# Kernel tuning notes

Hardware: AMD Instinct MI355X
Metric: run time of the kernel (lower is better)

The kernel has to match this reference:

```python
import jax, jax.numpy as jnp
import numpy as np

K_BINS = 8192
HIDDEN = 2048
SQRT2 = 1.4142135623730951
LEAKY_SLOPE = 0.01
TMIN = 1e-10


def setup_inputs() -> dict:
    key = jax.random.key(0)
    k0, k1, k2 = jax.random.split(key, 3)
    D = 2 * K_BINS  # mu length so that cat([mu, t]) has 2K+1 features
    # positive mu keeps mu ** (gamma - 1/(1-gamma)) (a fractional power) finite
    mu = jax.random.uniform(k0, (D,), jnp.float32, 0.1, 1.0)
    t = jnp.array([0.5], jnp.float32)
    gamma = jnp.array([0.5], jnp.float32)  # 1/(1-gamma) = 2 -> integral exponent
    W1 = jax.random.normal(k1, (D + 1, HIDDEN), jnp.float32) * (1.0 / np.sqrt(D + 1))
    b1 = jnp.zeros((HIDDEN,), jnp.float32)
    W2 = jax.random.normal(k2, (HIDDEN, D), jnp.float32) * (1.0 / np.sqrt(HIDDEN))
    b2 = jnp.zeros((D,), jnp.float32)
    return {"mu": mu, "t": t, "gamma": gamma, "W1": W1, "b1": b1,
            "W2": W2, "b2": b2, "K": K_BINS}


def reference(mu, t, gamma, W1, b1, W2, b2, K):
    g = gamma[0]
    # --- NN(cat([mu, t])) -> (mu_epsilon, ln_sigma_epsilon), each [K] ---
    inp = jnp.concatenate([mu, t])                      # [2K+1]
    h = jax.nn.leaky_relu(inp @ W1 + b1, LEAKY_SLOPE)   # [hidden]
    out = h @ W2 + b2                                   # [2K]
    mu_eps, ln_sig = out[:K], out[K:]
    # --- mu_x / sigma_x (t < tmin branch folded in via where) ---
    p_mu = g - 1.0 / (1.0 - g)
    p_eps = 1.0 / (1.0 - g)
    mu_x_nn = jnp.power(mu[:K], p_mu) * jnp.power(mu_eps, p_eps)
    sigma_x_nn = jnp.power(1.0 - g, -0.5) * jnp.exp(0.5 * ln_sig)
    use_nn = t[0] >= TMIN
    mu_x = jnp.where(use_nn, mu_x_nn, jnp.zeros_like(mu_eps))     # [K]
    sigma_x = jnp.where(use_nn, sigma_x_nn, jnp.ones_like(mu_eps))  # [K]
    # --- vectorized discretised CDF differences over the (D_out, K) grid ---
    kk = jnp.arange(K, dtype=jnp.float32)
    kl = 2.0 * (kk - 1.0) / (K - 1.0)   # left bin edges  [K]
    kr = 2.0 * kk / (K - 1.0)           # right bin edges [K]

    def cdf(x):  # x: [K] edges -> G: [D_out, K]
        z = (x[None, :] - mu_x[:, None]) / (sigma_x[:, None] * SQRT2)
        F = 0.5 * (1.0 + jax.lax.erf(z))
        return jnp.where(x[None, :] <= -1.0, 0.0,
                         jnp.where(x[None, :] >= 1.0, 1.0, F))

    return cdf(kr) - cdf(kl)  # [K, K] per-bin probabilities
```

## Files before the change

### kernel.cpp

```cpp
#include <hip/hip_runtime.h>
#include <math.h>

#define KBINS 8192
#define DDIM  16384
#define HID   2048
#define LASTROW 16384

#define C1 8
#define NCH1 2048

static constexpr float SQRT2_F  = 1.4142135623730951f;
static constexpr float INVSQ2PI = 0.3989422804014327f;

__device__ __forceinline__ float fast_erff(float x) {
    float ax = fabsf(x);
    float t  = 1.0f / fmaf(0.3275911f, ax, 1.0f);
    float p  = t * (0.254829592f +
               t * (-0.284496736f +
               t * (1.421413741f +
               t * (-1.453152027f +
               t * 1.061405429f))));
    float r = 1.0f - p * __expf(-ax * ax);
    return copysignf(r, x);
}

__global__ void __launch_bounds__(256)
mv1_partial(const float* __restrict__ mu, const float* __restrict__ W1,
            float* __restrict__ part1) {
    __shared__ float a_s[C1];
    int r0 = blockIdx.x * C1;
    if (threadIdx.x < C1) a_s[threadIdx.x] = mu[r0 + threadIdx.x];
    __syncthreads();
    int c0 = threadIdx.x * 4;
    const float* wp = W1 + (size_t)r0 * HID;
    float4 acc0 = {0.f, 0.f, 0.f, 0.f};
    float4 acc1 = {0.f, 0.f, 0.f, 0.f};
#pragma unroll
    for (int k = 0; k < C1; ++k) {
        float a = a_s[k];
        const float4 w0 = *reinterpret_cast<const float4*>(wp + (size_t)k * HID + c0);
        const float4 w1 = *reinterpret_cast<const float4*>(wp + (size_t)k * HID + c0 + 1024);
        acc0.x += a * w0.x; acc0.y += a * w0.y; acc0.z += a * w0.z; acc0.w += a * w0.w;
        acc1.x += a * w1.x; acc1.y += a * w1.y; acc1.z += a * w1.z; acc1.w += a * w1.w;
    }
    float* pp = part1 + (size_t)blockIdx.x * HID;
    *reinterpret_cast<float4*>(pp + c0)        = acc0;
    *reinterpret_cast<float4*>(pp + c0 + 1024) = acc1;
}

__global__ void __launch_bounds__(256)
h_reduce(const float* __restrict__ part1, const float* __restrict__ b1,
         const float* __restrict__ W1, const float* __restrict__ t,
         float* __restrict__ h) {
    __shared__ float red[32][9];
    int col_l = threadIdx.x & 7;
    int sub   = threadIdx.x >> 3;
    int c0    = blockIdx.x * 8;
    float s = 0.f;
    const float* p = part1 + c0 + col_l;
#pragma unroll 8
    for (int m = 0; m < 64; ++m)
        s += p[(size_t)(sub + (m << 5)) * HID];
    red[sub][col_l] = s;
    __syncthreads();
    if (threadIdx.x < 8) {
        int c = c0 + threadIdx.x;
        float v = b1[c] + t[0] * W1[(size_t)LASTROW * HID + c];
#pragma unroll
        for (int q = 0; q < 32; ++q) v += red[q][threadIdx.x];
        h[c] = (v >= 0.f) ? v : 0.01f * v;
    }
}

__global__ void __launch_bounds__(256)
fused_out(const float* __restrict__ h, const float* __restrict__ W2,
          const float* __restrict__ b2, const float* __restrict__ mu,
          const float* __restrict__ t, const float* __restrict__ gamma,
          float* __restrict__ out) {
    __shared__ float hs[HID];
    __shared__ float red[4][64];
    __shared__ float s01[2][32];
    __shared__ float sA[32], sB[32], sCf[32], sEr[32];
    const int tid = threadIdx.x;
    const int i0  = blockIdx.x * 32;

    for (int q = tid; q < HID; q += 256) hs[q] = h[q];
    __syncthreads();

    {
        int col_l = tid & 63;
        int chunk = tid >> 6;
        int c = i0 + (col_l & 31) + (col_l >> 5) * KBINS;
        const float* wp = W2 + c;
        int rbeg = chunk * 512;
        float s = 0.f;
#pragma unroll 16
        for (int r = rbeg; r < rbeg + 512; ++r)
            s += hs[r] * wp[(size_t)r * DDIM];
        red[chunk][col_l] = s;
    }
    __syncthreads();
    if (tid < 64) {
        int cl = tid & 31, hf = tid >> 5;
        float v = b2[i0 + cl + hf * KBINS]
                + red[0][tid] + red[1][tid] + red[2][tid] + red[3][tid];
        s01[hf][cl] = v;
    }
    __syncthreads();
    if (tid < 32) {
        float s0 = s01[0][tid];
        float s1 = s01[1][tid];
        float g  = gamma[0];
        float pe = 1.0f / (1.0f - g);
        float pm = g - pe;
        bool use_nn = (t[0] >= 1e-10f);
        float mval = use_nn ? powf(mu[i0 + tid], pm) * powf(s0, pe) : 0.0f;
        float invs = use_nn ? powf(1.0f - g, 0.5f) * expf(-0.5f * s1) : 1.0f;
        const float sc = 2.0f / 8191.0f;
        float A = sc * invs;
        sA[tid]  = A;
        sB[tid]  = (-1.0f / 8191.0f - mval) * invs;
        sCf[tid] = INVSQ2PI * A;
        float z = (8190.0f / 8191.0f - mval) * invs * (1.0f / SQRT2_F);
        sEr[tid] = 0.5f * (1.0f - fast_erff(z));
    }
    __syncthreads();

    for (int rr = 0; rr < 32; ++rr) {
        float A    = sA[rr];
        float B    = sB[rr];
        float coef = sCf[rr];
        float er   = sEr[rr];
        float* orow = out + (size_t)(i0 + rr) * KBINS;
#pragma unroll
        for (int it = 0; it < 8; ++it) {
            int j0 = it * 1024 + tid * 4;
            float4 r;
            if (j0 < 4096) {
                float u0 = fmaf((float)j0, A, B);
                float u1 = u0 + A;
                float u2 = u1 + A;
                float u3 = u2 + A;
                r.x = coef * __expf(-0.5f * u0 * u0);
                r.y = coef * __expf(-0.5f * u1 * u1);
                r.z = coef * __expf(-0.5f * u2 * u2);
                r.w = coef * __expf(-0.5f * u3 * u3);
            } else if (j0 == 4096) {
                r.x = er;
                r.y = r.z = r.w = 0.f;
            } else {
                r.x = r.y = r.z = r.w = 0.f;
            }
            *reinterpret_cast<float4*>(orow + j0) = r;
        }
    }
}

extern "C" void kernel_launch(void* const* d_in, const int* in_sizes, int n_in,
                              void* d_out, int out_size, void* d_ws, size_t ws_size,
                              hipStream_t stream) {
    const float* mu    = (const float*)d_in[0];
    const float* t     = (const float*)d_in[1];
    const float* gamma = (const float*)d_in[2];
    const float* W1    = (const float*)d_in[3];
    const float* b1    = (const float*)d_in[4];
    const float* W2    = (const float*)d_in[5];
    const float* b2    = (const float*)d_in[6];
    float* out = (float*)d_out;

    float* ws    = (float*)d_ws;
    float* part1 = ws;
    float* h     = part1 + (size_t)NCH1 * HID;

    mv1_partial<<<dim3(NCH1), dim3(256), 0, stream>>>(mu, W1, part1);
    h_reduce   <<<dim3(256),  dim3(256), 0, stream>>>(part1, b1, W1, t, h);
    fused_out  <<<dim3(256),  dim3(256), 0, stream>>>(h, W2, b2, mu, t, gamma, out);
}
```

Before: 138.6 us.

## Split second matvec across K with coalesced W2 reads and finer CDF blocks

Moves the W2 matvec out of the CDF kernel into a split-K kernel that also computes the hidden activations per 8-row slice, reading W2 rows contiguously across 1024 blocks and writing partial sums. The CDF kernel then reduces these partials for 4 output rows per block over 2048 blocks. This targets the strided, low-parallelism W2 reads in the old fused kernel, at the cost of an extra partial-sum buffer round trip and redundant reduction of part1 per block.

```diff
diff --git a/kernel.cpp b/kernel.cpp
--- a/kernel.cpp
+++ b/kernel.cpp
@@ -8,6 +8,7 @@
 
 #define C1 8
 #define NCH1 2048
+#define NCH2 256
 
 static constexpr float SQRT2_F  = 1.4142135623730951f;
 static constexpr float INVSQ2PI = 0.3989422804014327f;
@@ -49,67 +50,87 @@
 }
 
 __global__ void __launch_bounds__(256)
-h_reduce(const float* __restrict__ part1, const float* __restrict__ b1,
-         const float* __restrict__ W1, const float* __restrict__ t,
-         float* __restrict__ h) {
-    __shared__ float red[32][9];
-    int col_l = threadIdx.x & 7;
-    int sub   = threadIdx.x >> 3;
-    int c0    = blockIdx.x * 8;
-    float s = 0.f;
-    const float* p = part1 + c0 + col_l;
+mv2h(const float* __restrict__ part1, const float* __restrict__ b1,
+     const float* __restrict__ W1, const float* __restrict__ t,
+     const float* __restrict__ W2, float* __restrict__ part2) {
+    __shared__ float red[32][8];
+    __shared__ float hs[8];
+    const int tid   = threadIdx.x;
+    const int r0    = blockIdx.y * 8;
+    const int cbase = blockIdx.x * 4096;
+    {
+        int cl  = tid & 7;
+        int sub = tid >> 3;
+        float s = 0.f;
+        const float* p = part1 + r0 + cl;
 #pragma unroll 8
-    for (int m = 0; m < 64; ++m)
-        s += p[(size_t)(sub + (m << 5)) * HID];
-    red[sub][col_l] = s;
+        for (int m = 0; m < 64; ++m)
+            s += p[(size_t)(sub + (m << 5)) * HID];
+        red[sub][cl] = s;
+    }
     __syncthreads();
-    if (threadIdx.x < 8) {
-        int c = c0 + threadIdx.x;
-        float v = b1[c] + t[0] * W1[(size_t)LASTROW * HID + c];
+    if (tid < 8) {
+        int r = r0 + tid;
+        float v = b1[r] + t[0] * W1[(size_t)LASTROW * HID + r];
 #pragma unroll
-        for (int q = 0; q < 32; ++q) v += red[q][threadIdx.x];
-        h[c] = (v >= 0.f) ? v : 0.01f * v;
+        for (int q = 0; q < 32; ++q) v += red[q][tid];
+        hs[tid] = (v >= 0.f) ? v : 0.01f * v;
     }
+    __syncthreads();
+    int c0 = cbase + tid * 4;
+    float4 acc[4];
+#pragma unroll
+    for (int q = 0; q < 4; ++q) acc[q] = {0.f, 0.f, 0.f, 0.f};
+    const float* wp = W2 + (size_t)r0 * DDIM + c0;
+#pragma unroll 2
+    for (int k = 0; k < 8; ++k) {
+        float a = hs[k];
+        const float* wr = wp + (size_t)k * DDIM;
+#pragma unroll
+        for (int q = 0; q < 4; ++q) {
+            const float4 w = *reinterpret_cast<const float4*>(wr + q * 1024);
+            acc[q].x += a * w.x; acc[q].y += a * w.y;
+            acc[q].z += a * w.z; acc[q].w += a * w.w;
+        }
+    }
+    float* pp = part2 + (size_t)blockIdx.y * DDIM + c0;
+#pragma unroll
+    for (int q = 0; q < 4; ++q)
+        *reinterpret_cast<float4*>(pp + q * 1024) = acc[q];
 }
 
 __global__ void __launch_bounds__(256)
-fused_out(const float* __restrict__ h, const float* __restrict__ W2,
-          const float* __restrict__ b2, const float* __restrict__ mu,
-          const float* __restrict__ t, const float* __restrict__ gamma,
-          float* __restrict__ out) {
-    __shared__ float hs[HID];
-    __shared__ float red[4][64];
-    __shared__ float s01[2][32];
-    __shared__ float sA[32], sB[32], sCf[32], sEr[32];
+cdf_fused(const float* __restrict__ part2, const float* __restrict__ b2,
+          const float* __restrict__ mu, const float* __restrict__ t,
+          const float* __restrict__ gamma, float* __restrict__ out) {
+    __shared__ float red[32][8];
+    __shared__ float sv[8];
+    __shared__ float sA[4], sB[4], sCf[4], sEr[4];
     const int tid = threadIdx.x;
-    const int i0  = blockIdx.x * 32;
-
-    for (int q = tid; q < HID; q += 256) hs[q] = h[q];
-    __syncthreads();
-
+    const int i0  = blockIdx.x * 4;
     {
-        int col_l = tid & 63;
-        int chunk = tid >> 6;
-        int c = i0 + (col_l & 31) + (col_l >> 5) * KBINS;
-        const float* wp = W2 + c;
-        int rbeg = chunk * 512;
+        int col = tid & 7;
+        int sub = tid >> 3;
+        int gc  = (col < 4) ? (i0 + col) : (KBINS + i0 + col - 4);
         float s = 0.f;
-#pragma unroll 16
-        for (int r = rbeg; r < rbeg + 512; ++r)
-            s += hs[r] * wp[(size_t)r * DDIM];
-        red[chunk][col_l] = s;
+        const float* p = part2 + gc;
+#pragma unroll 8
+        for (int m = 0; m < 8; ++m)
+            s += p[(size_t)(sub + (m << 5)) * DDIM];
+        red[sub][col] = s;
     }
     __syncthreads();
-    if (tid < 64) {
-        int cl = tid & 31, hf = tid >> 5;
-        float v = b2[i0 + cl + hf * KBINS]
-                + red[0][tid] + red[1][tid] + red[2][tid] + red[3][tid];
-        s01[hf][cl] = v;
+    if (tid < 8) {
+        int gc = (tid < 4) ? (i0 + tid) : (KBINS + i0 + tid - 4);
+        float v = b2[gc];
+#pragma unroll
+        for (int q = 0; q < 32; ++q) v += red[q][tid];
+        sv[tid] = v;
     }
     __syncthreads();
-    if (tid < 32) {
-        float s0 = s01[0][tid];
-        float s1 = s01[1][tid];
+    if (tid < 4) {
+        float s0 = sv[tid];
+        float s1 = sv[tid + 4];
         float g  = gamma[0];
         float pe = 1.0f / (1.0f - g);
         float pm = g - pe;
@@ -125,8 +146,7 @@
         sEr[tid] = 0.5f * (1.0f - fast_erff(z));
     }
     __syncthreads();
-
-    for (int rr = 0; rr < 32; ++rr) {
+    for (int rr = 0; rr < 4; ++rr) {
         float A    = sA[rr];
         float B    = sB[rr];
         float coef = sCf[rr];
@@ -170,9 +190,9 @@
 
     float* ws    = (float*)d_ws;
     float* part1 = ws;
-    float* h     = part1 + (size_t)NCH1 * HID;
+    float* part2 = part1 + (size_t)NCH1 * HID;
 
-    mv1_partial<<<dim3(NCH1), dim3(256), 0, stream>>>(mu, W1, part1);
-    h_reduce   <<<dim3(256),  dim3(256), 0, stream>>>(part1, b1, W1, t, h);
-    fused_out  <<<dim3(256),  dim3(256), 0, stream>>>(h, W2, b2, mu, t, gamma, out);
+    mv1_partial<<<dim3(NCH1),    dim3(256), 0, stream>>>(mu, W1, part1);
+    mv2h       <<<dim3(4, NCH2), dim3(256), 0, stream>>>(part1, b1, W1, t, W2, part2);
+    cdf_fused  <<<dim3(2048),    dim3(256), 0, stream>>>(part2, b2, mu, t, gamma, out);
 }
```

After: 163.6 us. 1.18x slower.
